# Kernel tuning notes

Hardware: AMD Instinct MI355X
Metric: run time of the kernel (lower is better)

Reference implementation:

```python
import jax, jax.numpy as jnp
import numpy as np

B, N, E = 4, 8192, 131072
NODE_F, EDGE_F, HID, ACT = 16, 1, 128, 8


def _glorot(key, shape):
    fan_in, fan_out = shape[0], shape[1]
    lim = np.sqrt(6.0 / (fan_in + fan_out))
    return jax.random.uniform(key, shape, jnp.float32, -lim, lim)


def setup_inputs() -> dict:
    key = jax.random.key(0)
    ks = jax.random.split(key, 20)
    inp = {
        'node_features': jax.random.randint(ks[0], (B, N, NODE_F), 0, 10, jnp.int32),
        'edge_index': jax.random.randint(ks[1], (B, 2, E), 0, N, jnp.int64),
        'edge_features': jax.random.normal(ks[2], (B, E, EDGE_F), jnp.float32),
        # conv1: in = 2*NODE_F + EDGE_F
        'c1_w1': _glorot(ks[3], (2 * NODE_F + EDGE_F, HID)), 'c1_b1': jnp.zeros((HID,), jnp.float32),
        'c1_w2': _glorot(ks[4], (HID, HID)), 'c1_b2': jnp.zeros((HID,), jnp.float32),
        # conv2/conv3: in = 2*HID + 1
        'c2_w1': _glorot(ks[5], (2 * HID + 1, HID)), 'c2_b1': jnp.zeros((HID,), jnp.float32),
        'c2_w2': _glorot(ks[6], (HID, HID)), 'c2_b2': jnp.zeros((HID,), jnp.float32),
        'c3_w1': _glorot(ks[7], (2 * HID + 1, HID)), 'c3_b1': jnp.zeros((HID,), jnp.float32),
        'c3_w2': _glorot(ks[8], (HID, HID)), 'c3_b2': jnp.zeros((HID,), jnp.float32),
        'lin_w': _glorot(ks[9], (NODE_F + HID, ACT)), 'lin_b': jnp.zeros((ACT,), jnp.float32),
    }
    return inp


def _edge_conv(x, src, dst, ea, w1, b1, w2, b2):
    # message: cat([x_i (target), x_j (source), edge_attr]) -> Linear -> LeakyReLU -> Linear
    m = jnp.concatenate([x[dst], x[src], ea], axis=1)          # [E, 2F+EF]
    m = jax.nn.leaky_relu(m @ w1 + b1) @ w2 + b2               # [E, out]
    out = jax.ops.segment_min(m, dst, num_segments=x.shape[0])  # min-aggregate at targets
    cnt = jnp.zeros((x.shape[0],), m.dtype).at[dst].add(1.0)
    return jnp.where(cnt[:, None] > 0, out, 0.0)                # nodes w/o in-edges -> 0 (PyG)


def _graph_fwd(x0, ei, ea, p):
    x0 = x0.astype(jnp.float32)  # torch casts to IntTensor then MLP promotes; math on integer values
    src, dst = ei[0], ei[1]      # flow='source_to_target'
    x = jax.nn.leaky_relu(_edge_conv(x0, src, dst, ea, p['c1_w1'], p['c1_b1'], p['c1_w2'], p['c1_b2']))
    x = jax.nn.leaky_relu(_edge_conv(x, src, dst, ea, p['c2_w1'], p['c2_b1'], p['c2_w2'], p['c2_b2']))
    x = jax.nn.leaky_relu(_edge_conv(x, src, dst, ea, p['c3_w1'], p['c3_b1'], p['c3_w2'], p['c3_b2']))
    x = jnp.concatenate([x0, x], axis=1)
    return jax.nn.softplus(x @ p['lin_w'] + p['lin_b'])         # [N, ACT]


def reference(node_features, edge_index, edge_features,
              c1_w1, c1_b1, c1_w2, c1_b2,
              c2_w1, c2_b1, c2_w2, c2_b2,
              c3_w1, c3_b1, c3_w2, c3_b2,
              lin_w, lin_b):
    p = dict(c1_w1=c1_w1, c1_b1=c1_b1, c1_w2=c1_w2, c1_b2=c1_b2,
             c2_w1=c2_w1, c2_b1=c2_b1, c2_w2=c2_w2, c2_b2=c2_b2,
             c3_w1=c3_w1, c3_b1=c3_b1, c3_w2=c3_w2, c3_b2=c3_b2,
             lin_w=lin_w, lin_b=lin_b)
    return jax.vmap(lambda x, ei, ea: _graph_fwd(x, ei, ea, p))(
        node_features, edge_index, edge_features)               # [B, N, ACT]
```

## Files before the change

kernel.cpp:

```cpp
#include <hip/hip_runtime.h>

#define B_ 4
#define N_ 8192
#define E_ 131072
#define HID_ 128

typedef unsigned short us8 __attribute__((ext_vector_type(8)));
typedef unsigned short us4 __attribute__((ext_vector_type(4)));
typedef unsigned int   ui4 __attribute__((ext_vector_type(4)));
typedef int            i4  __attribute__((ext_vector_type(4)));
typedef __bf16         v8bf __attribute__((ext_vector_type(8)));
typedef float          v4f  __attribute__((ext_vector_type(4)));
typedef float          v2f  __attribute__((ext_vector_type(2)));

#define KEY_INF 0xFF800000u

__device__ __forceinline__ float b2f(unsigned short u) {
    return __uint_as_float(((unsigned)u) << 16);
}
__device__ __forceinline__ unsigned short f2b(float f) {
    unsigned x = __float_as_uint(f);
    return (unsigned short)((x + 0x7fffu + ((x >> 16) & 1u)) >> 16);
}
__device__ __forceinline__ unsigned fkey(float f) {
    unsigned b = __float_as_uint(f);
    return (b & 0x80000000u) ? ~b : (b | 0x80000000u);
}
__device__ __forceinline__ float funkey(unsigned k) {
    unsigned b = (k & 0x80000000u) ? (k ^ 0x80000000u) : ~k;
    return __uint_as_float(b);
}

__device__ __forceinline__ void repack_one(const float* __restrict__ w1, const float* __restrict__ w2,
                                           unsigned short* __restrict__ w1n, unsigned short* __restrict__ w2t,
                                           int F, int KPAD, int gid) {
    int t1 = 256 * KPAD;
    if (gid < t1) {
        int j = gid / KPAD, k = gid - j * KPAD;
        float v = 0.f;
        if (k < F) v = (j < 128) ? w1[k * 128 + j] : w1[(F + k) * 128 + (j - 128)];
        w1n[gid] = f2b(v);
    } else {
        int g = gid - t1;
        if (g < 16384) { int j = g >> 7, k = g & 127; w2t[g] = f2b(w2[k * 128 + j]); }
    }
}

__global__ void k_setup(const int* __restrict__ nf, unsigned short* __restrict__ x0b,
                        unsigned* __restrict__ cnt, unsigned* __restrict__ agg,
                        const float* __restrict__ w1a, const float* __restrict__ w2a,
                        const float* __restrict__ w1b, const float* __restrict__ w2b,
                        const float* __restrict__ w1c, const float* __restrict__ w2c,
                        unsigned short* __restrict__ w1n0, unsigned short* __restrict__ w2t0,
                        unsigned short* __restrict__ w1n1, unsigned short* __restrict__ w2t1,
                        unsigned short* __restrict__ w1n2, unsigned short* __restrict__ w2t2) {
    const int bid = blockIdx.x, tid = threadIdx.x;
    if (bid >= 4096) {
        const int rb = bid - 4096;
        const int gid = rb * 256 + tid;
        if (rb < 96)       repack_one(w1a, w2a, w1n0, w2t0, 16, 32, gid);
        else if (rb < 288) repack_one(w1b, w2b, w1n1, w2t1, 128, 128, gid - 96 * 256);
        else               repack_one(w1c, w2c, w1n2, w2t2, 128, 128, gid - 288 * 256);
        return;
    }
    const int gid = bid * 256 + tid;
    ui4 v = {KEY_INF, KEY_INF, KEY_INF, KEY_INF};
    ((ui4*)agg)[gid] = v;
    if (bid < 512) {
        i4 x = ((const i4*)nf)[gid];
        us4 o;
        o[0] = f2b((float)x[0]); o[1] = f2b((float)x[1]);
        o[2] = f2b((float)x[2]); o[3] = f2b((float)x[3]);
        ((us4*)x0b)[gid] = o;
    }
    if (bid < 128) cnt[gid] = 0u;
}

__global__ void k_hist(const int* __restrict__ ei, unsigned* __restrict__ cnt) {
    int gid = blockIdx.x * 256 + threadIdx.x;
    int b = gid >> 17, e = gid & (E_ - 1);
    int dst = ei[(b << 18) + E_ + e];
    atomicAdd(&cnt[(b << 13) + dst], 1u);
}

__global__ __launch_bounds__(1024) void k_scan(unsigned* __restrict__ cnt) {
    int b = blockIdx.x;
    __shared__ unsigned ps[1024];
    unsigned* c = cnt + (b << 13) + threadIdx.x * 8;
    unsigned loc[8]; unsigned s = 0;
#pragma unroll
    for (int i = 0; i < 8; i++) { loc[i] = c[i]; s += loc[i]; }
    ps[threadIdx.x] = s;
    __syncthreads();
    for (int off = 1; off < 1024; off <<= 1) {
        unsigned v = (threadIdx.x >= (unsigned)off) ? ps[threadIdx.x - off] : 0u;
        __syncthreads();
        ps[threadIdx.x] += v;
        __syncthreads();
    }
    unsigned run = ps[threadIdx.x] - s;
#pragma unroll
    for (int i = 0; i < 8; i++) { c[i] = run; run += loc[i]; }
}

__global__ void k_scatter(const int* __restrict__ ei, unsigned* __restrict__ wptr,
                          int* __restrict__ perm) {
    int gid = blockIdx.x * 256 + threadIdx.x;
    int b = gid >> 17, e = gid & (E_ - 1);
    int dst = ei[(b << 18) + E_ + e];
    unsigned pos = atomicAdd(&wptr[(b << 13) + dst], 1u);
    perm[(b << 17) + pos] = e;
}

template<int KPAD, bool FROM_AGG>
__global__ __launch_bounds__(256, 3) void k_node(
    const unsigned short* __restrict__ xin,
    unsigned* __restrict__ agg,
    const unsigned short* __restrict__ w1n,
    const float* __restrict__ bias1,
    unsigned short* __restrict__ Yd,
    unsigned short* __restrict__ Ys)
{
    constexpr int ASTR = KPAD + 8;
    __shared__ __align__(16) unsigned short A[64 * ASTR];
    __shared__ __align__(16) unsigned short Yb[64 * 264];

    const int tid = threadIdx.x;
    const int wave = tid >> 6, lane = tid & 63, lq = lane >> 4, lm = lane & 15;
    const int tile = (blockIdx.x & 7) * 64 + (blockIdx.x >> 3);
    const int n0 = tile * 64;

    v8bf wf[4][KPAD / 32]; float b1v[4];
#pragma unroll
    for (int nt = 0; nt < 4; nt++) {
        const int col = wave * 64 + nt * 16 + lm;
#pragma unroll
        for (int ks = 0; ks < KPAD / 32; ks++)
            wf[nt][ks] = *(const v8bf*)&w1n[col * KPAD + ks * 32 + lq * 8];
        b1v[nt] = (col < 128) ? bias1[col] : 0.f;
    }

    {
        const int row = tid >> 2, p = tid & 3;
        if (FROM_AGG) {
#pragma unroll
            for (int i = 0; i < 8; i++) {
                const int c = p + 4 * i;
                unsigned* ap = agg + ((size_t)(n0 + row)) * 128 + c * 4;
                ui4 k = *(ui4*)ap;
                ui4 inf = {KEY_INF, KEY_INF, KEY_INF, KEY_INF};
                *(ui4*)ap = inf;
                us4 o;
#pragma unroll
                for (int j = 0; j < 4; j++) {
                    float v = (k[j] == KEY_INF) ? 0.f : funkey(k[j]);
                    v = (v > 0.f) ? v : 0.01f * v;
                    o[j] = f2b(v);
                }
                *(us4*)&A[row * ASTR + c * 4] = o;
            }
        } else {
            us4 v = *(const us4*)(xin + ((size_t)(n0 + row)) * 16 + p * 4);
            *(us4*)&A[row * ASTR + p * 4] = v;
            us4 z = {0, 0, 0, 0};
            *(us4*)&A[row * ASTR + 16 + p * 4] = z;
        }
    }
    __syncthreads();

#pragma unroll
    for (int mt = 0; mt < 4; mt++) {
        v4f acc[4];
#pragma unroll
        for (int nt = 0; nt < 4; nt++) acc[nt] = v4f{0.f, 0.f, 0.f, 0.f};
#pragma unroll
        for (int ks = 0; ks < KPAD / 32; ks++) {
            v8bf a = *(const v8bf*)&A[(mt * 16 + lm) * ASTR + ks * 32 + lq * 8];
#pragma unroll
            for (int nt = 0; nt < 4; nt++)
                acc[nt] = __builtin_amdgcn_mfma_f32_16x16x32_bf16(a, wf[nt][ks], acc[nt], 0, 0, 0);
        }
#pragma unroll
        for (int nt = 0; nt < 4; nt++) {
            const int col = wave * 64 + nt * 16 + lm;
#pragma unroll
            for (int r = 0; r < 4; r++)
                Yb[(mt * 16 + lq * 4 + r) * 264 + col] = f2b(acc[nt][r] + b1v[nt]);
        }
    }
    __syncthreads();

    const int bb = tile >> 7, nl0 = (tile & 127) * 64;
#pragma unroll
    for (int i = 0; i < 8; i++) {
        const int idx = tid + 256 * i;
        const int row = idx >> 5, c = idx & 31;
        us8 v = *(const us8*)&Yb[row * 264 + c * 8];
        const int col0 = c * 8;
        unsigned short* dp = (col0 < 128)
            ? (Yd + ((size_t)(bb * N_) + nl0 + row) * 128 + col0)
            : (Ys + ((size_t)(bb * N_) + nl0 + row) * 128 + (col0 - 128));
        *(us8*)dp = v;
    }
}

__global__ __launch_bounds__(256, 4) void k_edge(
    const unsigned short* __restrict__ Yd,
    const unsigned short* __restrict__ Ys,
    const int* __restrict__ ei,
    const float* __restrict__ eaf,
    const int* __restrict__ perm,
    const unsigned short* __restrict__ w2t,
    const float* __restrict__ weap,
    const float* __restrict__ bias2,
    unsigned* __restrict__ agg)
{
    __shared__ __align__(16) unsigned short Hs[2][64 * 128];
    __shared__ __align__(16) int   dstl[2][64];
    __shared__ __align__(16) float weal[128];

    const int tid = threadIdx.x;
    const int wave = tid >> 6, lane = tid & 63, lq = lane >> 4, lm = lane & 15;

    if (tid < 128) weal[tid] = weap[tid];

    v8bf w2f[2][4]; float b2v[2];
#pragma unroll
    for (int nt = 0; nt < 2; nt++) {
        const int col = wave * 32 + nt * 16 + lm;
#pragma unroll
        for (int ks = 0; ks < 4; ks++)
            w2f[nt][ks] = *(const v8bf*)&w2t[col * 128 + ks * 32 + lq * 8];
        b2v[nt] = bias2[col];
    }

    const int arow = tid >> 2, p = tid & 3;
    const int s = ((arow & 0x0C) << 2) | ((arow >> 2) & 0x0C) | (arow & 3);
    const int rsw = arow & 15;

    int t = (blockIdx.x & 7) * 1024 + (blockIdx.x >> 3);
    int b = t >> 11;
    int e = perm[(b << 17) + (t & 2047) * 64 + s];
    int src = ei[(b << 18) + e];
    int dst = ei[(b << 18) + E_ + e];
    float ea = eaf[(b << 17) + e];

    {
        const ui4* ydp = (const ui4*)(Yd + ((size_t)(b * N_) + dst) * 128);
        const ui4* ysp = (const ui4*)(Ys + ((size_t)(b * N_) + src) * 128);
        if (p == 0) dstl[0][s] = dst;
        const v2f eav2 = {ea, ea};
        const v2f c01  = {0.01f, 0.01f};
        ui4 va = ydp[p], vb = ysp[p];
#pragma unroll
        for (int i = 0; i < 4; i++) {
            ui4 na, nb;
            if (i < 3) { na = ydp[p + 4 * (i + 1)]; nb = ysp[p + 4 * (i + 1)]; }
            const int c = p + 4 * i;
            ui4 od;
#pragma unroll
            for (int k = 0; k < 4; k++) {
                v2f a, bb2, z;
                a[0]   = __uint_as_float(va[k] << 16);
                a[1]   = __uint_as_float(va[k] & 0xffff0000u);
                bb2[0] = __uint_as_float(vb[k] << 16);
                bb2[1] = __uint_as_float(vb[k] & 0xffff0000u);
                v2f wv = *(const v2f*)&weal[c * 8 + 2 * k];
                z = a + bb2 + wv * eav2;
                z = __builtin_elementwise_max(z, z * c01);
                od[k] = __builtin_amdgcn_perm(__float_as_uint(z[1]) + 0x8000u,
                                              __float_as_uint(z[0]) + 0x8000u,
                                              0x07060302u);
            }
            *(ui4*)&Hs[0][arow * 128 + ((c ^ rsw) * 8)] = od;
            va = na; vb = nb;
        }
    }
    __syncthreads();

    for (int jj = 0; jj < 8; jj++) {
        const int curb = b, buf = jj & 1;

        t += 128;
        if (jj < 7) {
            b = t >> 11;
            e = perm[(b << 17) + (t & 2047) * 64 + s];
            src = ei[(b << 18) + e];
            dst = ei[(b << 18) + E_ + e];
            ea = eaf[(b << 17) + e];
        }

        {
            const int col0 = wave * 32 + lm, col1 = col0 + 16;
            unsigned* aggb = agg + (size_t)(curb * N_) * 128;
            float cur0 = 0.f, cur1 = 0.f; int curd = -1;
#pragma unroll
            for (int mt = 0; mt < 4; mt++) {
                const int row = mt * 16 + lm;
                v4f acc0 = {b2v[0], b2v[0], b2v[0], b2v[0]};
                v4f acc1 = {b2v[1], b2v[1], b2v[1], b2v[1]};
#pragma unroll
                for (int ks = 0; ks < 4; ks++) {
                    v8bf a = *(const v8bf*)&Hs[buf][row * 128 + (((ks * 4 + lq) ^ lm) * 8)];
                    acc0 = __builtin_amdgcn_mfma_f32_16x16x32_bf16(a, w2f[0][ks], acc0, 0, 0, 0);
                    acc1 = __builtin_amdgcn_mfma_f32_16x16x32_bf16(a, w2f[1][ks], acc1, 0, 0, 0);
                }
                i4 dv = *(const i4*)&dstl[buf][lq * 16 + mt * 4];
#pragma unroll
                for (int r = 0; r < 4; r++) {
                    const float v0 = acc0[r];
                    const float v1 = acc1[r];
                    const int d = dv[r];
                    if (d != curd) {
                        if (curd >= 0) {
                            atomicMin(aggb + (size_t)curd * 128 + col0, fkey(cur0));
                            atomicMin(aggb + (size_t)curd * 128 + col1, fkey(cur1));
                        }
                        curd = d; cur0 = v0; cur1 = v1;
                    } else {
                        cur0 = fminf(cur0, v0); cur1 = fminf(cur1, v1);
                    }
                }
            }
            atomicMin(aggb + (size_t)curd * 128 + col0, fkey(cur0));
            atomicMin(aggb + (size_t)curd * 128 + col1, fkey(cur1));
        }

        if (jj < 7) {
            const ui4* ydp = (const ui4*)(Yd + ((size_t)(b * N_) + dst) * 128);
            const ui4* ysp = (const ui4*)(Ys + ((size_t)(b * N_) + src) * 128);
            if (p == 0) dstl[buf ^ 1][s] = dst;
            const v2f eav2 = {ea, ea};
            const v2f c01  = {0.01f, 0.01f};
            ui4 va = ydp[p], vb = ysp[p];
#pragma unroll
            for (int i = 0; i < 4; i++) {
                ui4 na, nb;
                if (i < 3) { na = ydp[p + 4 * (i + 1)]; nb = ysp[p + 4 * (i + 1)]; }
                const int c = p + 4 * i;
                ui4 od;
#pragma unroll
                for (int k = 0; k < 4; k++) {
                    v2f a, bb2, z;
                    a[0]   = __uint_as_float(va[k] << 16);
                    a[1]   = __uint_as_float(va[k] & 0xffff0000u);
                    bb2[0] = __uint_as_float(vb[k] << 16);
                    bb2[1] = __uint_as_float(vb[k] & 0xffff0000u);
                    v2f wv = *(const v2f*)&weal[c * 8 + 2 * k];
                    z = a + bb2 + wv * eav2;
                    z = __builtin_elementwise_max(z, z * c01);
                    od[k] = __builtin_amdgcn_perm(__float_as_uint(z[1]) + 0x8000u,
                                                  __float_as_uint(z[0]) + 0x8000u,
                                                  0x07060302u);
                }
                *(ui4*)&Hs[buf ^ 1][arow * 128 + ((c ^ rsw) * 8)] = od;
                va = na; vb = nb;
            }
        }
        __syncthreads();
    }
}

__global__ __launch_bounds__(256, 4) void k_final(
    const unsigned short* __restrict__ x0b, const unsigned* __restrict__ agg,
    const float* __restrict__ lw, const float* __restrict__ lb,
    float* __restrict__ out) {
    __shared__ float w[144 * 8];
    __shared__ float bias8[8];
    __shared__ float xs[64 * 129];
    const int tid = threadIdx.x;
    for (int i = tid; i < 1152; i += 256) w[i] = lw[i];
    if (tid < 8) bias8[tid] = lb[tid];
    const int n0 = blockIdx.x * 64;
#pragma unroll
    for (int i = 0; i < 8; i++) {
        const int idx = tid + 256 * i;
        const int row = idx >> 5, c = idx & 31;
        ui4 k = ((const ui4*)(agg + ((size_t)(n0 + row)) * 128))[c];
#pragma unroll
        for (int j = 0; j < 4; j++) {
            float v = (k[j] == KEY_INF) ? 0.f : funkey(k[j]);
            v = fmaxf(v, 0.01f * v);
            xs[row * 129 + c * 4 + j] = v;
        }
    }
    __syncthreads();
    const int node = tid >> 2, ap = (tid & 3) * 2;
    float a0 = bias8[ap], a1 = bias8[ap + 1];
    const unsigned short* x0 = x0b + (size_t)(n0 + node) * 16;
#pragma unroll
    for (int f = 0; f < 16; f++) {
        const float xv = b2f(x0[f]);
        a0 += xv * w[f * 8 + ap]; a1 += xv * w[f * 8 + ap + 1];
    }
    const float* xr = &xs[node * 129];
#pragma unroll 8
    for (int f = 0; f < 128; f++) {
        const float xv = xr[f];
        a0 += xv * w[(16 + f) * 8 + ap]; a1 += xv * w[(16 + f) * 8 + ap + 1];
    }
    v2f o;
    o[0] = fmaxf(a0, 0.f) + log1pf(expf(-fabsf(a0)));
    o[1] = fmaxf(a1, 0.f) + log1pf(expf(-fabsf(a1)));
    *(v2f*)&out[(size_t)(n0 + node) * 8 + ap] = o;
}

extern "C" void kernel_launch(void* const* d_in, const int* in_sizes, int n_in,
                              void* d_out, int out_size, void* d_ws, size_t ws_size,
                              hipStream_t stream) {
    (void)in_sizes; (void)n_in; (void)out_size; (void)ws_size;
    const int* nf  = (const int*)d_in[0];
    const int* ei  = (const int*)d_in[1];
    const float* eaf = (const float*)d_in[2];
    const float* cw1[3] = {(const float*)d_in[3],  (const float*)d_in[7],  (const float*)d_in[11]};
    const float* cb1[3] = {(const float*)d_in[4],  (const float*)d_in[8],  (const float*)d_in[12]};
    const float* cw2[3] = {(const float*)d_in[5],  (const float*)d_in[9],  (const float*)d_in[13]};
    const float* cb2[3] = {(const float*)d_in[6],  (const float*)d_in[10], (const float*)d_in[14]};
    const float* lw = (const float*)d_in[15];
    const float* lb = (const float*)d_in[16];
    float* out = (float*)d_out;

    size_t off = 0;
    auto carve = [&](size_t bytes) { void* p = (char*)d_ws + off; off += (bytes + 255) & ~(size_t)255; return p; };
    unsigned short* x0b  = (unsigned short*)carve((size_t)B_ * N_ * 16 * 2);
    unsigned*       agg  = (unsigned*)carve((size_t)B_ * N_ * 128 * 4);
    unsigned*       cnt  = (unsigned*)carve((size_t)B_ * N_ * 4);
    int*            perm = (int*)carve((size_t)B_ * E_ * 4);
    unsigned short* Yd   = (unsigned short*)carve((size_t)B_ * N_ * 128 * 2);
    unsigned short* Ys   = (unsigned short*)carve((size_t)B_ * N_ * 128 * 2);
    unsigned short* w1n0 = (unsigned short*)carve(256 * 32 * 2);
    unsigned short* w2t0 = (unsigned short*)carve(128 * 128 * 2);
    unsigned short* w1n1 = (unsigned short*)carve(256 * 128 * 2);
    unsigned short* w2t1 = (unsigned short*)carve(128 * 128 * 2);
    unsigned short* w1n2 = (unsigned short*)carve(256 * 128 * 2);
    unsigned short* w2t2 = (unsigned short*)carve(128 * 128 * 2);

    k_setup<<<4576, 256, 0, stream>>>(nf, x0b, cnt, agg,
                                      cw1[0], cw2[0], cw1[1], cw2[1], cw1[2], cw2[2],
                                      w1n0, w2t0, w1n1, w2t1, w1n2, w2t2);
    k_hist<<<2048, 256, 0, stream>>>(ei, cnt);
    k_scan<<<B_, 1024, 0, stream>>>(cnt);
    k_scatter<<<2048, 256, 0, stream>>>(ei, cnt, perm);

    k_node<32, false><<<512, 256, 0, stream>>>(x0b, agg, w1n0, cb1[0], Yd, Ys);
    k_edge<<<1024, 256, 0, stream>>>(Yd, Ys, ei, eaf, perm, w2t0, cw1[0] + 32 * 128, cb2[0], agg);

    k_node<128, true><<<512, 256, 0, stream>>>(x0b, agg, w1n1, cb1[1], Yd, Ys);
    k_edge<<<1024, 256, 0, stream>>>(Yd, Ys, ei, eaf, perm, w2t1, cw1[1] + 256 * 128, cb2[1], agg);

    k_node<128, true><<<512, 256, 0, stream>>>(x0b, agg, w1n2, cb1[2], Yd, Ys);
    k_edge<<<1024, 256, 0, stream>>>(Yd, Ys, ei, eaf, perm, w2t2, cw1[2] + 256 * 128, cb2[2], agg);

    k_final<<<512, 256, 0, stream>>>(x0b, agg, lw, lb, out);
}
```

Measured before the change: 306.2 us.

## Switch edge-stage intermediates to fp16 packed math and fuse scatter with first node GEMM

Node-stage outputs Yd/Ys and the edge hidden tile are now stored as fp16 instead of bf16. This lets the edge kernel do the add, edge-feature FMA and leaky-ReLU in packed half math, with no per-element unpack to fp32 and repack, and it feeds f16 MFMA with fp16 W2. Separately, the permutation scatter kernel and the first node GEMM are merged into one launch to remove a kernel boundary. The fp16 path trades bf16 range for precision and could overflow on large activations; the fused launch also gives up the ordering between scatter and node1, which is fine because they are independent.

```diff
diff --git a/kernel.cpp b/kernel.cpp
--- a/kernel.cpp
+++ b/kernel.cpp
@@ -10,6 +10,7 @@
 typedef unsigned int   ui4 __attribute__((ext_vector_type(4)));
 typedef int            i4  __attribute__((ext_vector_type(4)));
 typedef __bf16         v8bf __attribute__((ext_vector_type(8)));
+typedef _Float16       hf8 __attribute__((ext_vector_type(8)));
 typedef float          v4f  __attribute__((ext_vector_type(4)));
 typedef float          v2f  __attribute__((ext_vector_type(2)));
 
@@ -21,6 +22,9 @@
 __device__ __forceinline__ unsigned short f2b(float f) {
     unsigned x = __float_as_uint(f);
     return (unsigned short)((x + 0x7fffu + ((x >> 16) & 1u)) >> 16);
+}
+__device__ __forceinline__ unsigned short f2h(float f) {
+    union { _Float16 h; unsigned short u; } c; c.h = (_Float16)f; return c.u;
 }
 __device__ __forceinline__ unsigned fkey(float f) {
     unsigned b = __float_as_uint(f);
@@ -42,7 +46,7 @@
         w1n[gid] = f2b(v);
     } else {
         int g = gid - t1;
-        if (g < 16384) { int j = g >> 7, k = g & 127; w2t[g] = f2b(w2[k * 128 + j]); }
+        if (g < 16384) { int j = g >> 7, k = g & 127; w2t[g] = f2h(w2[k * 128 + j]); }
     }
 }
 
@@ -103,31 +107,24 @@
     for (int i = 0; i < 8; i++) { c[i] = run; run += loc[i]; }
 }
 
-__global__ void k_scatter(const int* __restrict__ ei, unsigned* __restrict__ wptr,
-                          int* __restrict__ perm) {
-    int gid = blockIdx.x * 256 + threadIdx.x;
-    int b = gid >> 17, e = gid & (E_ - 1);
-    int dst = ei[(b << 18) + E_ + e];
-    unsigned pos = atomicAdd(&wptr[(b << 13) + dst], 1u);
-    perm[(b << 17) + pos] = e;
-}
-
 template<int KPAD, bool FROM_AGG>
-__global__ __launch_bounds__(256, 3) void k_node(
+__device__ __forceinline__ void node_body(
+    int bid,
     const unsigned short* __restrict__ xin,
     unsigned* __restrict__ agg,
     const unsigned short* __restrict__ w1n,
     const float* __restrict__ bias1,
     unsigned short* __restrict__ Yd,
-    unsigned short* __restrict__ Ys)
+    unsigned short* __restrict__ Ys,
+    char* smem)
 {
     constexpr int ASTR = KPAD + 8;
-    __shared__ __align__(16) unsigned short A[64 * ASTR];
-    __shared__ __align__(16) unsigned short Yb[64 * 264];
+    unsigned short* A  = (unsigned short*)smem;
+    unsigned short* Yb = (unsigned short*)(smem + 64 * ASTR * 2);
 
     const int tid = threadIdx.x;
     const int wave = tid >> 6, lane = tid & 63, lq = lane >> 4, lm = lane & 15;
-    const int tile = (blockIdx.x & 7) * 64 + (blockIdx.x >> 3);
+    const int tile = (bid & 7) * 64 + (bid >> 3);
     const int n0 = tile * 64;
 
     v8bf wf[4][KPAD / 32]; float b1v[4];
@@ -185,7 +182,7 @@
             const int col = wave * 64 + nt * 16 + lm;
 #pragma unroll
             for (int r = 0; r < 4; r++)
-                Yb[(mt * 16 + lq * 4 + r) * 264 + col] = f2b(acc[nt][r] + b1v[nt]);
+                Yb[(mt * 16 + lq * 4 + r) * 264 + col] = f2h(acc[nt][r] + b1v[nt]);
         }
     }
     __syncthreads();
@@ -202,6 +199,35 @@
             : (Ys + ((size_t)(bb * N_) + nl0 + row) * 128 + (col0 - 128));
         *(us8*)dp = v;
     }
+}
+
+template<int KPAD>
+__global__ __launch_bounds__(256, 3) void k_node(
+    const unsigned short* __restrict__ xin, unsigned* __restrict__ agg,
+    const unsigned short* __restrict__ w1n, const float* __restrict__ bias1,
+    unsigned short* __restrict__ Yd, unsigned short* __restrict__ Ys)
+{
+    __shared__ __align__(16) char smem[64 * (KPAD + 8) * 2 + 64 * 264 * 2];
+    node_body<KPAD, true>(blockIdx.x, xin, agg, w1n, bias1, Yd, Ys, smem);
+}
+
+__global__ __launch_bounds__(256, 3) void k_scat_node1(
+    const int* __restrict__ ei, unsigned* __restrict__ wptr, int* __restrict__ perm,
+    const unsigned short* __restrict__ x0b,
+    const unsigned short* __restrict__ w1n, const float* __restrict__ bias1,
+    unsigned short* __restrict__ Yd, unsigned short* __restrict__ Ys)
+{
+    __shared__ __align__(16) char smem[64 * 40 * 2 + 64 * 264 * 2];
+    const int bid = blockIdx.x;
+    if (bid < 2048) {
+        int gid = bid * 256 + threadIdx.x;
+        int b = gid >> 17, e = gid & (E_ - 1);
+        int dst = ei[(b << 18) + E_ + e];
+        unsigned pos = atomicAdd(&wptr[(b << 13) + dst], 1u);
+        perm[(b << 17) + pos] = e;
+        return;
+    }
+    node_body<32, false>(bid - 2048, x0b, (unsigned*)nullptr, w1n, bias1, Yd, Ys, smem);
 }
 
 __global__ __launch_bounds__(256, 4) void k_edge(
@@ -216,27 +242,31 @@
     unsigned* __restrict__ agg)
 {
     __shared__ __align__(16) unsigned short Hs[2][64 * 128];
-    __shared__ __align__(16) int   dstl[2][64];
-    __shared__ __align__(16) float weal[128];
+    __shared__ __align__(16) int      dstl[2][64];
+    __shared__ __align__(16) _Float16 weal[128];
 
     const int tid = threadIdx.x;
     const int wave = tid >> 6, lane = tid & 63, lq = lane >> 4, lm = lane & 15;
 
-    if (tid < 128) weal[tid] = weap[tid];
-
-    v8bf w2f[2][4]; float b2v[2];
+    if (tid < 128) weal[tid] = (_Float16)weap[tid];
+
+    hf8 w2f[2][4]; float b2v[2];
 #pragma unroll
     for (int nt = 0; nt < 2; nt++) {
         const int col = wave * 32 + nt * 16 + lm;
 #pragma unroll
         for (int ks = 0; ks < 4; ks++)
-            w2f[nt][ks] = *(const v8bf*)&w2t[col * 128 + ks * 32 + lq * 8];
+            w2f[nt][ks] = *(const hf8*)&w2t[col * 128 + ks * 32 + lq * 8];
         b2v[nt] = bias2[col];
     }
+    __syncthreads();
 
     const int arow = tid >> 2, p = tid & 3;
     const int s = ((arow & 0x0C) << 2) | ((arow >> 2) & 0x0C) | (arow & 3);
     const int rsw = arow & 15;
+
+    const hf8 c01v = {(_Float16)0.01f, (_Float16)0.01f, (_Float16)0.01f, (_Float16)0.01f,
+                      (_Float16)0.01f, (_Float16)0.01f, (_Float16)0.01f, (_Float16)0.01f};
 
     int t = (blockIdx.x & 7) * 1024 + (blockIdx.x >> 3);
     int b = t >> 11;
@@ -246,33 +276,21 @@
     float ea = eaf[(b << 17) + e];
 
     {
-        const ui4* ydp = (const ui4*)(Yd + ((size_t)(b * N_) + dst) * 128);
-        const ui4* ysp = (const ui4*)(Ys + ((size_t)(b * N_) + src) * 128);
+        const hf8* ydp = (const hf8*)(Yd + ((size_t)(b * N_) + dst) * 128);
+        const hf8* ysp = (const hf8*)(Ys + ((size_t)(b * N_) + src) * 128);
         if (p == 0) dstl[0][s] = dst;
-        const v2f eav2 = {ea, ea};
-        const v2f c01  = {0.01f, 0.01f};
-        ui4 va = ydp[p], vb = ysp[p];
+        const _Float16 eh = (_Float16)ea;
+        const hf8 ea8 = {eh, eh, eh, eh, eh, eh, eh, eh};
+        hf8 va = ydp[p], vb = ysp[p];
 #pragma unroll
         for (int i = 0; i < 4; i++) {
-            ui4 na, nb;
+            hf8 na, nb;
             if (i < 3) { na = ydp[p + 4 * (i + 1)]; nb = ysp[p + 4 * (i + 1)]; }
             const int c = p + 4 * i;
-            ui4 od;
-#pragma unroll
-            for (int k = 0; k < 4; k++) {
-                v2f a, bb2, z;
-                a[0]   = __uint_as_float(va[k] << 16);
-                a[1]   = __uint_as_float(va[k] & 0xffff0000u);
-                bb2[0] = __uint_as_float(vb[k] << 16);
-                bb2[1] = __uint_as_float(vb[k] & 0xffff0000u);
-                v2f wv = *(const v2f*)&weal[c * 8 + 2 * k];
-                z = a + bb2 + wv * eav2;
-                z = __builtin_elementwise_max(z, z * c01);
-                od[k] = __builtin_amdgcn_perm(__float_as_uint(z[1]) + 0x8000u,
-                                              __float_as_uint(z[0]) + 0x8000u,
-                                              0x07060302u);
-            }
-            *(ui4*)&Hs[0][arow * 128 + ((c ^ rsw) * 8)] = od;
+            hf8 wv = *(const hf8*)&weal[c * 8];
+            hf8 z = va + vb + wv * ea8;
+            z = __builtin_elementwise_max(z, z * c01v);
+            *(hf8*)&Hs[0][arow * 128 + ((c ^ rsw) * 8)] = z;
             va = na; vb = nb;
         }
     }
@@ -301,9 +319,9 @@
                 v4f acc1 = {b2v[1], b2v[1], b2v[1], b2v[1]};
 #pragma unroll
                 for (int ks = 0; ks < 4; ks++) {
-                    v8bf a = *(const v8bf*)&Hs[buf][row * 128 + (((ks * 4 + lq) ^ lm) * 8)];
-                    acc0 = __builtin_amdgcn_mfma_f32_16x16x32_bf16(a, w2f[0][ks], acc0, 0, 0, 0);
-                    acc1 = __builtin_amdgcn_mfma_f32_16x16x32_bf16(a, w2f[1][ks], acc1, 0, 0, 0);
+                    hf8 a = *(const hf8*)&Hs[buf][row * 128 + (((ks * 4 + lq) ^ lm) * 8)];
+                    acc0 = __builtin_amdgcn_mfma_f32_16x16x32_f16(a, w2f[0][ks], acc0, 0, 0, 0);
+                    acc1 = __builtin_amdgcn_mfma_f32_16x16x32_f16(a, w2f[1][ks], acc1, 0, 0, 0);
                 }
                 i4 dv = *(const i4*)&dstl[buf][lq * 16 + mt * 4];
 #pragma unroll
@@ -327,33 +345,21 @@
         }
 
         if (jj < 7) {
-            const ui4* ydp = (const ui4*)(Yd + ((size_t)(b * N_) + dst) * 128);
-            const ui4* ysp = (const ui4*)(Ys + ((size_t)(b * N_) + src) * 128);
+            const hf8* ydp = (const hf8*)(Yd + ((size_t)(b * N_) + dst) * 128);
+            const hf8* ysp = (const hf8*)(Ys + ((size_t)(b * N_) + src) * 128);
             if (p == 0) dstl[buf ^ 1][s] = dst;
-            const v2f eav2 = {ea, ea};
-            const v2f c01  = {0.01f, 0.01f};
-            ui4 va = ydp[p], vb = ysp[p];
+            const _Float16 eh = (_Float16)ea;
+            const hf8 ea8 = {eh, eh, eh, eh, eh, eh, eh, eh};
+            hf8 va = ydp[p], vb = ysp[p];
 #pragma unroll
             for (int i = 0; i < 4; i++) {
-                ui4 na, nb;
+                hf8 na, nb;
                 if (i < 3) { na = ydp[p + 4 * (i + 1)]; nb = ysp[p + 4 * (i + 1)]; }
                 const int c = p + 4 * i;
-                ui4 od;
-#pragma unroll
-                for (int k = 0; k < 4; k++) {
-                    v2f a, bb2, z;
-                    a[0]   = __uint_as_float(va[k] << 16);
-                    a[1]   = __uint_as_float(va[k] & 0xffff0000u);
-                    bb2[0] = __uint_as_float(vb[k] << 16);
-                    bb2[1] = __uint_as_float(vb[k] & 0xffff0000u);
-                    v2f wv = *(const v2f*)&weal[c * 8 + 2 * k];
-                    z = a + bb2 + wv * eav2;
-                    z = __builtin_elementwise_max(z, z * c01);
-                    od[k] = __builtin_amdgcn_perm(__float_as_uint(z[1]) + 0x8000u,
-                                                  __float_as_uint(z[0]) + 0x8000u,
-                                                  0x07060302u);
-                }
-                *(ui4*)&Hs[buf ^ 1][arow * 128 + ((c ^ rsw) * 8)] = od;
+                hf8 wv = *(const hf8*)&weal[c * 8];
+                hf8 z = va + vb + wv * ea8;
+                z = __builtin_elementwise_max(z, z * c01v);
+                *(hf8*)&Hs[buf ^ 1][arow * 128 + ((c ^ rsw) * 8)] = z;
                 va = na; vb = nb;
             }
         }
@@ -440,15 +446,14 @@
                                       w1n0, w2t0, w1n1, w2t1, w1n2, w2t2);
     k_hist<<<2048, 256, 0, stream>>>(ei, cnt);
     k_scan<<<B_, 1024, 0, stream>>>(cnt);
-    k_scatter<<<2048, 256, 0, stream>>>(ei, cnt, perm);
-
-    k_node<32, false><<<512, 256, 0, stream>>>(x0b, agg, w1n0, cb1[0], Yd, Ys);
+
+    k_scat_node1<<<2560, 256, 0, stream>>>(ei, cnt, perm, x0b, w1n0, cb1[0], Yd, Ys);
     k_edge<<<1024, 256, 0, stream>>>(Yd, Ys, ei, eaf, perm, w2t0, cw1[0] + 32 * 128, cb2[0], agg);
 
-    k_node<128, true><<<512, 256, 0, stream>>>(x0b, agg, w1n1, cb1[1], Yd, Ys);
+    k_node<128><<<512, 256, 0, stream>>>(x0b, agg, w1n1, cb1[1], Yd, Ys);
     k_edge<<<1024, 256, 0, stream>>>(Yd, Ys, ei, eaf, perm, w2t1, cw1[1] + 256 * 128, cb2[1], agg);
 
-    k_node<128, true><<<512, 256, 0, stream>>>(x0b, agg, w1n2, cb1[2], Yd, Ys);
+    k_node<128><<<512, 256, 0, stream>>>(x0b, agg, w1n2, cb1[2], Yd, Ys);
     k_edge<<<1024, 256, 0, stream>>>(Yd, Ys, ei, eaf, perm, w2t2, cw1[2] + 256 * 128, cb2[2], agg);
 
     k_final<<<512, 256, 0, stream>>>(x0b, agg, lw, lb, out);
```

Result: faster. 297.5 us, median of 2 (-2.9%).
